# Optimization experiments

Hardware: AMD Instinct MI355X
Metric: run time of the kernel (lower is better)

Reference implementation:

```python
import jax, jax.numpy as jnp
import numpy as np

B, L, T = 256, 1024, 128

def setup_inputs() -> dict:
    key = jax.random.key(0)
    k1, k2, k3, k4 = jax.random.split(key, 4)
    inputs = jax.random.normal(k1, (B, L, T), dtype=jnp.float32)
    tag_indices = jax.random.randint(k2, (B, L), 0, T, dtype=jnp.int64)
    sequence_lengths = jax.random.randint(k3, (B,), 1, L + 1, dtype=jnp.int64)
    # xavier-ish scale for transitions
    transition_params = jax.random.normal(k4, (T, T), dtype=jnp.float32) * (2.0 / (T + T)) ** 0.5
    return {"inputs": inputs, "tag_indices": tag_indices,
            "sequence_lengths": sequence_lengths, "transition_params": transition_params}

def _crf_log_likelihood(inputs, tag_indices, sequence_lengths, transition_params):
    b, l, t = inputs.shape
    mask = (jnp.arange(l)[None, :] < sequence_lengths[:, None]).astype(inputs.dtype)  # [B,L]

    # --- unary score: sum_t inputs[b, t, tag[b,t]] over valid t ---
    unary = jnp.take_along_axis(inputs, tag_indices[:, :, None], axis=2)[:, :, 0]  # [B,L]
    unary_score = jnp.sum(unary * mask, axis=1)

    # --- binary score: sum_t trans[tag[t], tag[t+1]] masked by mask[:,1:] ---
    trans_sc = transition_params[tag_indices[:, :-1], tag_indices[:, 1:]]  # [B,L-1]
    binary_score = jnp.sum(trans_sc * mask[:, 1:], axis=1)
    sequence_scores = unary_score + binary_score

    # --- log normalizer via forward algorithm (log-space scan) ---
    first = inputs[:, 0]                               # [B,T]
    rest = jnp.transpose(inputs[:, 1:], (1, 0, 2))     # [L-1,B,T]

    def step(state, inp_t):
        # state: [B,T] previous alphas; transition broadcast: [B,T_prev,T_next]
        new = inp_t + jax.nn.logsumexp(state[:, :, None] + transition_params[None], axis=1)
        return new, new

    _, alphas = jax.lax.scan(step, first, rest)        # [L-1,B,T]
    # original indexes all_alphas at max(0, seq_len - 2)
    idx = jnp.clip(sequence_lengths - 2, 0, l - 2)
    final_alphas = alphas[idx, jnp.arange(b)]          # [B,T]
    log_norm = jax.nn.logsumexp(final_alphas, axis=1)
    log_norm = jnp.where(sequence_lengths <= 0, jnp.zeros_like(log_norm), log_norm)

    return sequence_scores - log_norm

def reference(inputs, tag_indices, sequence_lengths, transition_params):
    return _crf_log_likelihood(inputs, tag_indices, sequence_lengths, transition_params)
```

## Files before the change

### kernel.cpp

```cpp
#include <hip/hip_runtime.h>


#define B_   256
#define LL   1024
#define TT   128
#define NBLK 16
#define L2E  1.4426950408889634f
#define LN2f 0.6931471805599453f

typedef __attribute__((ext_vector_type(8))) short bf16x8;
typedef __attribute__((ext_vector_type(4))) float f32x4;
union bfrw { unsigned w[4]; bf16x8 v; };

__device__ __forceinline__ unsigned bfround(float x) {
    unsigned u = __float_as_uint(x);
    return u + 0x7fffu + ((u >> 16) & 1u);
}
__device__ __forceinline__ unsigned pack2(float lo, float hi) {
#if __has_builtin(__builtin_amdgcn_cvt_pk_bf16_f32)
    auto p = __builtin_amdgcn_cvt_pk_bf16_f32(lo, hi);
    unsigned w; __builtin_memcpy(&w, &p, 4); return w;
#else
    return __builtin_amdgcn_perm(bfround(hi), bfround(lo), 0x07060302);
#endif
}
__device__ __forceinline__ void lds_barrier() {
    asm volatile("s_waitcnt lgkmcnt(0)\n\ts_barrier" ::: "memory");
}

template<bool FWD, int PH>
__device__ __forceinline__ void phase(int t, float& Dacc, float4 (&up)[4][2],
                                      const bf16x8 (&af)[2][4],
                                      short* qls, float* sb, const float* pu,
                                      float* __restrict__ qcap, float* __restrict__ rcap,
                                      float* __restrict__ dqv, float* __restrict__ drv,
                                      int cb, int tfin, int rank,
                                      int wid, int quad, int bl)
{
    constexpr int CUR  = PH & 1;
    constexpr int NXT  = CUR ^ 1;
    constexpr int SLOT = FWD ? ((1 + PH) & 3) : ((3 - PH) & 3);

    bfrw bfr[4];
    #pragma unroll
    for (int c = 0; c < 4; ++c)
        bfr[c].v = *(const bf16x8*)(qls + CUR * (16 * 136) + bl * 136 + (4 * c + quad) * 8);
    float sprev = sb[CUR * 16 + bl];
    float ci = __builtin_amdgcn_rcpf(sprev);

    f32x4 ae0 = {0.f,0.f,0.f,0.f}, ao0 = {0.f,0.f,0.f,0.f};
    f32x4 ae1 = {0.f,0.f,0.f,0.f}, ao1 = {0.f,0.f,0.f,0.f};
    ae0 = __builtin_amdgcn_mfma_f32_16x16x32_bf16(af[0][0], bfr[0].v, ae0, 0, 0, 0);
    ae1 = __builtin_amdgcn_mfma_f32_16x16x32_bf16(af[1][0], bfr[0].v, ae1, 0, 0, 0);
    ao0 = __builtin_amdgcn_mfma_f32_16x16x32_bf16(af[0][1], bfr[1].v, ao0, 0, 0, 0);
    ao1 = __builtin_amdgcn_mfma_f32_16x16x32_bf16(af[1][1], bfr[1].v, ao1, 0, 0, 0);
    ae0 = __builtin_amdgcn_mfma_f32_16x16x32_bf16(af[0][2], bfr[2].v, ae0, 0, 0, 0);
    ae1 = __builtin_amdgcn_mfma_f32_16x16x32_bf16(af[1][2], bfr[2].v, ae1, 0, 0, 0);
    ao0 = __builtin_amdgcn_mfma_f32_16x16x32_bf16(af[0][3], bfr[3].v, ao0, 0, 0, 0);
    ao1 = __builtin_amdgcn_mfma_f32_16x16x32_bf16(af[1][3], bfr[3].v, ao1, 0, 0, 0);

    float ex[8];
    #pragma unroll
    for (int mt = 0; mt < 2; ++mt) {
        float4 v = up[SLOT][mt];
        ex[4*mt+0] = __builtin_amdgcn_exp2f(v.x * L2E);
        ex[4*mt+1] = __builtin_amdgcn_exp2f(v.y * L2E);
        ex[4*mt+2] = __builtin_amdgcn_exp2f(v.z * L2E);
        ex[4*mt+3] = __builtin_amdgcn_exp2f(v.w * L2E);
    }
    {
        int tp = FWD ? (t + 4) : (t - 5);
        tp = tp < 0 ? 0 : (tp > LL - 1 ? LL - 1 : tp);
        #pragma unroll
        for (int mt = 0; mt < 2; ++mt)
            up[SLOT][mt] = *(const float4*)(pu + (size_t)tp * TT + mt * 16);
    }
    Dacc += __builtin_amdgcn_logf(sprev);

    f32x4 s0v = ae0 + ao0;
    f32x4 s1v = ae1 + ao1;

    float rv[8];
    #pragma unroll
    for (int r = 0; r < 4; ++r) { rv[r] = ci * s0v[r]; rv[4 + r] = ci * s1v[r]; }

    if (!FWD) {
        bool cap = (cb == t - 1) && (cb != tfin);
        if (__any(cap)) {
            if (cap) {
                float4 c0 = {rv[0], rv[1], rv[2], rv[3]};
                float4 c1 = {rv[4], rv[5], rv[6], rv[7]};
                *(float4*)(rcap + rank * TT + wid * 32 + quad * 4) = c0;
                *(float4*)(rcap + rank * TT + wid * 32 + 16 + quad * 4) = c1;
                if (wid == 0 && quad == 0) drv[rank] = Dacc;
            }
        }
        bool inj = (tfin == t - 1);
        #pragma unroll
        for (int k = 0; k < 8; ++k) rv[k] = inj ? 1.0f : rv[k];
        Dacc = inj ? 0.0f : Dacc;
    }

    float ov[8];
    #pragma unroll
    for (int k = 0; k < 8; ++k) ov[k] = ex[k] * rv[k];

    if (FWD) {
        bool cap = (cb == t);
        if (__any(cap)) {
            if (cap) {
                float4 c0 = {ov[0], ov[1], ov[2], ov[3]};
                float4 c1 = {ov[4], ov[5], ov[6], ov[7]};
                *(float4*)(qcap + rank * TT + wid * 32 + quad * 4) = c0;
                *(float4*)(qcap + rank * TT + wid * 32 + 16 + quad * 4) = c1;
                if (wid == 0 && quad == 0) dqv[rank] = Dacc;
            }
        }
    }

    if (wid == 0 && quad == 0) sb[NXT * 16 + bl] = s0v[0];

    bfrw pk;
    pk.w[0] = pack2(ov[0], ov[1]);
    pk.w[1] = pack2(ov[2], ov[3]);
    pk.w[2] = pack2(ov[4], ov[5]);
    pk.w[3] = pack2(ov[6], ov[7]);
    *(bf16x8*)(qls + NXT * (16 * 136) + bl * 136 + (4 * wid + quad) * 8) = pk.v;

    lds_barrier();
}

__launch_bounds__(256, 1)
__global__ void crf_scan(const float* __restrict__ inputs,
                         const int*   __restrict__ tags,
                         const int*   __restrict__ slens,
                         const float* __restrict__ trans,
                         float* __restrict__ qcap, float* __restrict__ rcap,
                         float* __restrict__ dqv,  float* __restrict__ drv,
                         int* __restrict__ perm, float* __restrict__ scorebuf)
{
    __shared__ __align__(16) short qls[2 * 16 * 136];
    __shared__ float sb[2 * 16];
    __shared__ int keys[B_];

    const int tid  = threadIdx.x;

    if (blockIdx.x >= 2 * NBLK) {
        const int sbid = blockIdx.x - 2 * NBLK;
        const int lane = tid & 63, wid = tid >> 6;
        #pragma unroll 1
        for (int bi = 0; bi < 4; ++bi) {
            const int b = sbid * 4 + bi;
            const int slen = slens[b];
            const float* inb  = inputs + (size_t)b * LL * TT;
            const int*   tagb = tags + b * LL;
            float sc = 0.f;
            for (int t = tid; t < slen; t += 256) {
                int tg = tagb[t];
                float v = inb[(size_t)t * TT + tg];
                if (t >= 1) v += trans[tagb[t - 1] * TT + tg];
                sc += v;
            }
            #pragma unroll
            for (int off = 32; off > 0; off >>= 1) sc += __shfl_xor(sc, off, 64);
            if (lane == 0) sb[wid] = sc;
            __syncthreads();
            if (tid == 0) scorebuf[b] = sb[0] + sb[1] + sb[2] + sb[3];
            __syncthreads();
        }
        return;
    }

    const int lane = tid & 63;
    const int wid  = __builtin_amdgcn_readfirstlane(tid >> 6);
    const int quad = lane >> 4;
    const int bl   = lane & 15;
    const bool isf = (blockIdx.x < NBLK);
    const int g    = isf ? blockIdx.x : blockIdx.x - NBLK;

    keys[tid] = slens[tid] * 256 + tid;
    __syncthreads();
    for (int k = 2; k <= B_; k <<= 1) {
        for (int s = k >> 1; s > 0; s >>= 1) {
            int ixj = tid ^ s;
            if (ixj > tid) {
                int a = keys[tid], b2 = keys[ixj];
                bool asc = ((tid & k) == 0);
                if ((a > b2) == asc) { keys[tid] = b2; keys[ixj] = a; }
            }
            __syncthreads();
        }
    }
    if (isf && tid < 16) perm[g * 16 + tid] = keys[g * 16 + tid] & 255;

    const int key = keys[g * 16 + bl];
    const int ob  = key & 255;
    const int sl  = key >> 8;
    int tfin = sl - 1; if (tfin < 1) tfin = 1;

    int tmax = tfin;
    #pragma unroll
    for (int o = 1; o < 16; o <<= 1) {
        int c2 = __shfl_xor(tmax, o, 16); tmax = c2 > tmax ? c2 : tmax;
    }
    tmax = __builtin_amdgcn_readfirstlane(tmax);

    const int C  = (tmax + 4) >> 1;
    const int cb = tfin < C ? tfin : C;

    int cmax = cb, cmin = cb;
    #pragma unroll
    for (int o = 1; o < 16; o <<= 1) {
        int a = __shfl_xor(cmax, o, 16); cmax = a > cmax ? a : cmax;
        int b2 = __shfl_xor(cmin, o, 16); cmin = b2 < cmin ? b2 : cmin;
    }
    cmax = __builtin_amdgcn_readfirstlane(cmax);
    cmin = __builtin_amdgcn_readfirstlane(cmin);

    bf16x8 af[2][4];
    #pragma unroll
    for (int mt = 0; mt < 2; ++mt) {
        const int j = wid * 32 + mt * 16 + bl;
        #pragma unroll
        for (int c = 0; c < 4; ++c) {
            #pragma unroll
            for (int jj = 0; jj < 8; ++jj) {
                int k = 32 * c + 16 * (jj >> 2) + 4 * quad + (jj & 3);
                int idx = isf ? (k * TT + j) : (j * TT + k);
                float ev = __builtin_amdgcn_exp2f(trans[idx] * L2E);
                af[mt][c][jj] = (short)(bfround(ev) >> 16);
            }
        }
    }

    const float* pu = inputs + (size_t)ob * LL * TT + wid * 32 + quad * 4;
    const int rank = g * 16 + bl;
    float Dacc = 0.f;
    float4 up[4][2];

    if (tid < 16) sb[tid] = 1.0f;

    if (isf) {
        float q0[8];
        #pragma unroll
        for (int mt = 0; mt < 2; ++mt) {
            float4 v = *(const float4*)(pu + mt * 16);
            q0[4*mt+0] = __builtin_amdgcn_exp2f(v.x * L2E);
            q0[4*mt+1] = __builtin_amdgcn_exp2f(v.y * L2E);
            q0[4*mt+2] = __builtin_amdgcn_exp2f(v.z * L2E);
            q0[4*mt+3] = __builtin_amdgcn_exp2f(v.w * L2E);
        }
        bfrw pk;
        pk.w[0] = pack2(q0[0], q0[1]);
        pk.w[1] = pack2(q0[2], q0[3]);
        pk.w[2] = pack2(q0[4], q0[5]);
        pk.w[3] = pack2(q0[6], q0[7]);
        *(bf16x8*)(qls + bl * 136 + (4 * wid + quad) * 8) = pk.v;

        #pragma unroll
        for (int s = 1; s <= 4; ++s) {
            #pragma unroll
            for (int mt = 0; mt < 2; ++mt)
                up[s & 3][mt] = *(const float4*)(pu + (size_t)s * TT + mt * 16);
        }
        __syncthreads();

        for (int tb = 1; tb <= cmax; tb += 4) {
            phase<true,0>(tb+0, Dacc, up, af, qls, sb, pu, qcap, rcap, dqv, drv, cb, tfin, rank, wid, quad, bl);
            phase<true,1>(tb+1, Dacc, up, af, qls, sb, pu, qcap, rcap, dqv, drv, cb, tfin, rank, wid, quad, bl);
            phase<true,2>(tb+2, Dacc, up, af, qls, sb, pu, qcap, rcap, dqv, drv, cb, tfin, rank, wid, quad, bl);
            phase<true,3>(tb+3, Dacc, up, af, qls, sb, pu, qcap, rcap, dqv, drv, cb, tfin, rank, wid, quad, bl);
        }
    } else {
        bfrw pk;
        pk.w[0] = pk.w[1] = pk.w[2] = pk.w[3] = 0x3F803F80u;
        *(bf16x8*)(qls + bl * 136 + (4 * wid + quad) * 8) = pk.v;
        if (cb == tfin) {
            float4 one4 = {1.f, 1.f, 1.f, 1.f};
            *(float4*)(rcap + rank * TT + wid * 32 + quad * 4) = one4;
            *(float4*)(rcap + rank * TT + wid * 32 + 16 + quad * 4) = one4;
            if (wid == 0 && quad == 0) drv[rank] = 0.f;
        }

        const int tb0 = (tmax + 4) & ~3;
        #pragma unroll
        for (int ph = 0; ph < 4; ++ph) {
            int ui = tb0 - 1 - ph;
            ui = ui > LL - 1 ? LL - 1 : (ui < 0 ? 0 : ui);
            #pragma unroll
            for (int mt = 0; mt < 2; ++mt)
                up[(3 - ph) & 3][mt] = *(const float4*)(pu + (size_t)ui * TT + mt * 16);
        }
        __syncthreads();

        for (int tb = tb0; tb > cmin; tb -= 4) {
            phase<false,0>(tb-0, Dacc, up, af, qls, sb, pu, qcap, rcap, dqv, drv, cb, tfin, rank, wid, quad, bl);
            phase<false,1>(tb-1, Dacc, up, af, qls, sb, pu, qcap, rcap, dqv, drv, cb, tfin, rank, wid, quad, bl);
            phase<false,2>(tb-2, Dacc, up, af, qls, sb, pu, qcap, rcap, dqv, drv, cb, tfin, rank, wid, quad, bl);
            phase<false,3>(tb-3, Dacc, up, af, qls, sb, pu, qcap, rcap, dqv, drv, cb, tfin, rank, wid, quad, bl);
        }
    }
}

__global__ void crf_comb(const float* __restrict__ qcap, const float* __restrict__ rcap,
                         const float* __restrict__ dqv, const float* __restrict__ drv,
                         const int* __restrict__ perm, const float* __restrict__ scorebuf,
                         float* __restrict__ out) {
    const int tid = threadIdx.x;
    const int r16 = tid >> 4, part = tid & 15;
    const int rank = blockIdx.x * 16 + r16;
    const float* qc = qcap + rank * TT + part * 8;
    const float* rc = rcap + rank * TT + part * 8;
    float4 a0 = *(const float4*)(qc);
    float4 a1 = *(const float4*)(qc + 4);
    float4 b0 = *(const float4*)(rc);
    float4 b1 = *(const float4*)(rc + 4);
    float s = a0.x*b0.x + a0.y*b0.y + a0.z*b0.z + a0.w*b0.w
            + a1.x*b1.x + a1.y*b1.y + a1.z*b1.z + a1.w*b1.w;
    #pragma unroll
    for (int o = 1; o < 16; o <<= 1) s += __shfl_xor(s, o, 16);
    if (part == 0) {
        int ob = perm[rank];
        float logZ = LN2f * (__builtin_amdgcn_logf(s) + dqv[rank] + drv[rank]);
        out[ob] = scorebuf[ob] - logZ;
    }
}

extern "C" void kernel_launch(void* const* d_in, const int* in_sizes, int n_in,
                              void* d_out, int out_size, void* d_ws, size_t ws_size,
                              hipStream_t stream) {
    const float* inputs = (const float*)d_in[0];
    const int*   tags   = (const int*)d_in[1];
    const int*   slens  = (const int*)d_in[2];
    const float* trans  = (const float*)d_in[3];
    float* out = (float*)d_out;

    float* qcap = (float*)d_ws;
    float* rcap = qcap + 32768;
    float* dqv  = rcap + 32768;
    float* drv  = dqv + 256;
    int*   perm = (int*)(drv + 256);
    float* scorebuf = (float*)(perm + 256);

    crf_scan<<<2 * NBLK + 64, 256, 0, stream>>>(inputs, tags, slens, trans,
                                                qcap, rcap, dqv, drv, perm, scorebuf);
    crf_comb<<<NBLK, 256, 0, stream>>>(qcap, rcap, dqv, drv, perm, scorebuf, out);
}
```

Baseline: 410.3 us.

## Run one single-wave block per sequence with fp16 register matvec instead of MFMA

Replaces the 16-sequence-per-block MFMA scan, which needed a sort by length and a 4-wave LDS barrier every step, with 512 single-wavefront blocks, one per sequence and direction. Each lane keeps two columns of exp(transitions) as packed fp16 in registers and computes the matvec with scalar fp16-to-fp32 FMAs, so steps need only an LDS waitcnt and no s_barrier. Each block also stops at its own sequence's meet point rather than the group maximum. The score work is spread over 256 one-wave blocks. The cost is about 128 FMAs per lane per step on the vector ALUs instead of matrix cores, heavy register pressure from the 128-entry E array, and fp16 range and precision risk in the scaled alphas.

Result: slower. 743.9 us (+81.3%).

```diff
diff --git a/kernel.cpp b/kernel.cpp
--- a/kernel.cpp
+++ b/kernel.cpp
@@ -1,316 +1,232 @@
 #include <hip/hip_runtime.h>
 
 
-#define B_   256
 #define LL   1024
 #define TT   128
-#define NBLK 16
 #define L2E  1.4426950408889634f
 #define LN2f 0.6931471805599453f
 
-typedef __attribute__((ext_vector_type(8))) short bf16x8;
-typedef __attribute__((ext_vector_type(4))) float f32x4;
-union bfrw { unsigned w[4]; bf16x8 v; };
-
-__device__ __forceinline__ unsigned bfround(float x) {
-    unsigned u = __float_as_uint(x);
-    return u + 0x7fffu + ((u >> 16) & 1u);
-}
-__device__ __forceinline__ unsigned pack2(float lo, float hi) {
-#if __has_builtin(__builtin_amdgcn_cvt_pk_bf16_f32)
-    auto p = __builtin_amdgcn_cvt_pk_bf16_f32(lo, hi);
-    unsigned w; __builtin_memcpy(&w, &p, 4); return w;
+typedef __attribute__((ext_vector_type(2))) __fp16 h2;
+typedef __attribute__((ext_vector_type(2))) float f2;
+union h2u { h2 h; unsigned u; };
+
+__device__ __forceinline__ h2 pkh(float lo, float hi) {
+#if __has_builtin(__builtin_amdgcn_cvt_pkrtz)
+    return __builtin_amdgcn_cvt_pkrtz(lo, hi);
 #else
-    return __builtin_amdgcn_perm(bfround(hi), bfround(lo), 0x07060302);
+    h2 r; r.x = (__fp16)lo; r.y = (__fp16)hi; return r;
 #endif
 }
-__device__ __forceinline__ void lds_barrier() {
-    asm volatile("s_waitcnt lgkmcnt(0)\n\ts_barrier" ::: "memory");
+__device__ __forceinline__ float dmix(h2 a, h2 b, float c) {
+    c += (float)a.x * (float)b.x;
+    c += (float)a.y * (float)b.y;
+    return c;
 }
 
 template<bool FWD, int PH>
-__device__ __forceinline__ void phase(int t, float& Dacc, float4 (&up)[4][2],
-                                      const bf16x8 (&af)[2][4],
-                                      short* qls, float* sb, const float* pu,
-                                      float* __restrict__ qcap, float* __restrict__ rcap,
-                                      float* __restrict__ dqv, float* __restrict__ drv,
-                                      int cb, int tfin, int rank,
-                                      int wid, int quad, int bl)
+__device__ __forceinline__ void step1(int t, float& Dacc, f2 (&up)[4],
+                                      const h2 (&E)[64][2],
+                                      unsigned (&lds)[2][128],
+                                      const float* pu,
+                                      float* capg, float* dcapg,
+                                      int cb, int tfin, int lane)
 {
     constexpr int CUR  = PH & 1;
     constexpr int NXT  = CUR ^ 1;
     constexpr int SLOT = FWD ? ((1 + PH) & 3) : ((3 - PH) & 3);
 
-    bfrw bfr[4];
-    #pragma unroll
-    for (int c = 0; c < 4; ++c)
-        bfr[c].v = *(const bf16x8*)(qls + CUR * (16 * 136) + bl * 136 + (4 * c + quad) * 8);
-    float sprev = sb[CUR * 16 + bl];
-    float ci = __builtin_amdgcn_rcpf(sprev);
-
-    f32x4 ae0 = {0.f,0.f,0.f,0.f}, ao0 = {0.f,0.f,0.f,0.f};
-    f32x4 ae1 = {0.f,0.f,0.f,0.f}, ao1 = {0.f,0.f,0.f,0.f};
-    ae0 = __builtin_amdgcn_mfma_f32_16x16x32_bf16(af[0][0], bfr[0].v, ae0, 0, 0, 0);
-    ae1 = __builtin_amdgcn_mfma_f32_16x16x32_bf16(af[1][0], bfr[0].v, ae1, 0, 0, 0);
-    ao0 = __builtin_amdgcn_mfma_f32_16x16x32_bf16(af[0][1], bfr[1].v, ao0, 0, 0, 0);
-    ao1 = __builtin_amdgcn_mfma_f32_16x16x32_bf16(af[1][1], bfr[1].v, ao1, 0, 0, 0);
-    ae0 = __builtin_amdgcn_mfma_f32_16x16x32_bf16(af[0][2], bfr[2].v, ae0, 0, 0, 0);
-    ae1 = __builtin_amdgcn_mfma_f32_16x16x32_bf16(af[1][2], bfr[2].v, ae1, 0, 0, 0);
-    ao0 = __builtin_amdgcn_mfma_f32_16x16x32_bf16(af[0][3], bfr[3].v, ao0, 0, 0, 0);
-    ao1 = __builtin_amdgcn_mfma_f32_16x16x32_bf16(af[1][3], bfr[3].v, ao1, 0, 0, 0);
-
-    float ex[8];
-    #pragma unroll
-    for (int mt = 0; mt < 2; ++mt) {
-        float4 v = up[SLOT][mt];
-        ex[4*mt+0] = __builtin_amdgcn_exp2f(v.x * L2E);
-        ex[4*mt+1] = __builtin_amdgcn_exp2f(v.y * L2E);
-        ex[4*mt+2] = __builtin_amdgcn_exp2f(v.z * L2E);
-        ex[4*mt+3] = __builtin_amdgcn_exp2f(v.w * L2E);
-    }
+    float sprev = __uint_as_float(lds[CUR][64]);
+    const uint4* sp = (const uint4*)&lds[CUR][0];
+
+    float ex0 = __builtin_amdgcn_exp2f(up[SLOT].x * L2E);
+    float ex1 = __builtin_amdgcn_exp2f(up[SLOT].y * L2E);
     {
         int tp = FWD ? (t + 4) : (t - 5);
         tp = tp < 0 ? 0 : (tp > LL - 1 ? LL - 1 : tp);
-        #pragma unroll
-        for (int mt = 0; mt < 2; ++mt)
-            up[SLOT][mt] = *(const float4*)(pu + (size_t)tp * TT + mt * 16);
-    }
-    Dacc += __builtin_amdgcn_logf(sprev);
-
-    f32x4 s0v = ae0 + ao0;
-    f32x4 s1v = ae1 + ao1;
-
-    float rv[8];
+        up[SLOT] = *(const f2*)(pu + (size_t)tp * TT);
+    }
+
+    float a[4] = {0.f, 0.f, 0.f, 0.f};
+    float c[4] = {0.f, 0.f, 0.f, 0.f};
     #pragma unroll
-    for (int r = 0; r < 4; ++r) { rv[r] = ci * s0v[r]; rv[4 + r] = ci * s1v[r]; }
+    for (int g = 0; g < 4; ++g) {
+        #pragma unroll
+        for (int r = 0; r < 4; ++r) {
+            uint4 wv = sp[4 * g + r];
+            const int k0 = g * 16 + r * 4;
+            h2u u0, u1, u2, u3;
+            u0.u = wv.x; u1.u = wv.y; u2.u = wv.z; u3.u = wv.w;
+            a[g] = dmix(E[k0+0][0], u0.h, a[g]);
+            c[g] = dmix(E[k0+0][1], u0.h, c[g]);
+            a[g] = dmix(E[k0+1][0], u1.h, a[g]);
+            c[g] = dmix(E[k0+1][1], u1.h, c[g]);
+            a[g] = dmix(E[k0+2][0], u2.h, a[g]);
+            c[g] = dmix(E[k0+2][1], u2.h, c[g]);
+            a[g] = dmix(E[k0+3][0], u3.h, a[g]);
+            c[g] = dmix(E[k0+3][1], u3.h, c[g]);
+        }
+    }
+    float s0 = (a[0] + a[1]) + (a[2] + a[3]);
+    float s1 = (c[0] + c[1]) + (c[2] + c[3]);
+
+    float ci = __builtin_amdgcn_rcpf(sprev);
+    float lg = __builtin_amdgcn_logf(sprev);
+    bool inj = (!FWD) && (tfin == t - 1);
+    float cis  = inj ? 0.f : ci;
+    float injf = inj ? 1.f : 0.f;
+    Dacc = inj ? 0.f : (Dacc + lg);
+
+    float rv0 = cis * s0 + injf;
+    float rv1 = cis * s1 + injf;
 
     if (!FWD) {
-        bool cap = (cb == t - 1) && (cb != tfin);
-        if (__any(cap)) {
-            if (cap) {
-                float4 c0 = {rv[0], rv[1], rv[2], rv[3]};
-                float4 c1 = {rv[4], rv[5], rv[6], rv[7]};
-                *(float4*)(rcap + rank * TT + wid * 32 + quad * 4) = c0;
-                *(float4*)(rcap + rank * TT + wid * 32 + 16 + quad * 4) = c1;
-                if (wid == 0 && quad == 0) drv[rank] = Dacc;
-            }
-        }
-        bool inj = (tfin == t - 1);
-        #pragma unroll
-        for (int k = 0; k < 8; ++k) rv[k] = inj ? 1.0f : rv[k];
-        Dacc = inj ? 0.0f : Dacc;
-    }
-
-    float ov[8];
-    #pragma unroll
-    for (int k = 0; k < 8; ++k) ov[k] = ex[k] * rv[k];
+        if (cb == t - 1 && cb != tfin) {
+            f2 cp; cp.x = rv0; cp.y = rv1;
+            *(f2*)(capg + 2 * lane) = cp;
+            if (lane == 0) *dcapg = Dacc;
+        }
+    }
+
+    float ov0 = ex0 * rv0;
+    float ov1 = ex1 * rv1;
 
     if (FWD) {
-        bool cap = (cb == t);
-        if (__any(cap)) {
-            if (cap) {
-                float4 c0 = {ov[0], ov[1], ov[2], ov[3]};
-                float4 c1 = {ov[4], ov[5], ov[6], ov[7]};
-                *(float4*)(qcap + rank * TT + wid * 32 + quad * 4) = c0;
-                *(float4*)(qcap + rank * TT + wid * 32 + 16 + quad * 4) = c1;
-                if (wid == 0 && quad == 0) dqv[rank] = Dacc;
-            }
-        }
-    }
-
-    if (wid == 0 && quad == 0) sb[NXT * 16 + bl] = s0v[0];
-
-    bfrw pk;
-    pk.w[0] = pack2(ov[0], ov[1]);
-    pk.w[1] = pack2(ov[2], ov[3]);
-    pk.w[2] = pack2(ov[4], ov[5]);
-    pk.w[3] = pack2(ov[6], ov[7]);
-    *(bf16x8*)(qls + NXT * (16 * 136) + bl * 136 + (4 * wid + quad) * 8) = pk.v;
-
-    lds_barrier();
-}
-
-__launch_bounds__(256, 1)
+        if (cb == t) {
+            f2 cp; cp.x = ov0; cp.y = ov1;
+            *(f2*)(capg + 2 * lane) = cp;
+            if (lane == 0) *dcapg = Dacc;
+        }
+    }
+
+    h2u pk; pk.h = pkh(ov0, ov1);
+    lds[NXT][lane] = pk.u;
+    if (lane == 0) lds[NXT][64] = __float_as_uint(s0);
+    asm volatile("s_waitcnt lgkmcnt(0)" ::: "memory");
+}
+
+__launch_bounds__(64, 1)
 __global__ void crf_scan(const float* __restrict__ inputs,
                          const int*   __restrict__ tags,
                          const int*   __restrict__ slens,
                          const float* __restrict__ trans,
                          float* __restrict__ qcap, float* __restrict__ rcap,
                          float* __restrict__ dqv,  float* __restrict__ drv,
-                         int* __restrict__ perm, float* __restrict__ scorebuf)
+                         float* __restrict__ scorebuf)
 {
-    __shared__ __align__(16) short qls[2 * 16 * 136];
-    __shared__ float sb[2 * 16];
-    __shared__ int keys[B_];
-
-    const int tid  = threadIdx.x;
-
-    if (blockIdx.x >= 2 * NBLK) {
-        const int sbid = blockIdx.x - 2 * NBLK;
-        const int lane = tid & 63, wid = tid >> 6;
+    const int bid  = blockIdx.x;
+    const int lane = threadIdx.x;
+
+    if (bid >= 512) {
+        const int b = bid - 512;
+        const int slen = slens[b];
+        const float* inb  = inputs + (size_t)b * LL * TT;
+        const int*   tagb = tags + b * LL;
+        float sc = 0.f;
+        for (int t = lane; t < slen; t += 64) {
+            int tg = tagb[t];
+            float v = inb[(size_t)t * TT + tg];
+            if (t >= 1) v += trans[tagb[t - 1] * TT + tg];
+            sc += v;
+        }
+        #pragma unroll
+        for (int off = 32; off > 0; off >>= 1) sc += __shfl_xor(sc, off, 64);
+        if (lane == 0) scorebuf[b] = sc;
+        return;
+    }
+
+    __shared__ __align__(16) unsigned lds[2][128];
+
+    const bool isf = bid < 256;
+    const int  b   = isf ? bid : bid - 256;
+
+    int sl = slens[b];
+    int tfin = sl - 1; if (tfin < 1) tfin = 1;
+    const int cb = (tfin + 1) >> 1;
+
+    h2 E[64][2];
+    if (isf) {
+        #pragma unroll
+        for (int kk = 0; kk < 64; ++kk) {
+            f2 r0 = *(const f2*)(trans + (size_t)(2 * kk)     * TT + 2 * lane);
+            f2 r1 = *(const f2*)(trans + (size_t)(2 * kk + 1) * TT + 2 * lane);
+            E[kk][0] = pkh(__builtin_amdgcn_exp2f(r0.x * L2E),
+                           __builtin_amdgcn_exp2f(r1.x * L2E));
+            E[kk][1] = pkh(__builtin_amdgcn_exp2f(r0.y * L2E),
+                           __builtin_amdgcn_exp2f(r1.y * L2E));
+        }
+    } else {
+        #pragma unroll
+        for (int jj = 0; jj < 64; ++jj) {
+            f2 r0 = *(const f2*)(trans + (size_t)(2 * lane)     * TT + 2 * jj);
+            f2 r1 = *(const f2*)(trans + (size_t)(2 * lane + 1) * TT + 2 * jj);
+            E[jj][0] = pkh(__builtin_amdgcn_exp2f(r0.x * L2E),
+                           __builtin_amdgcn_exp2f(r0.y * L2E));
+            E[jj][1] = pkh(__builtin_amdgcn_exp2f(r1.x * L2E),
+                           __builtin_amdgcn_exp2f(r1.y * L2E));
+        }
+    }
+
+    const float* pu = inputs + (size_t)b * LL * TT + 2 * lane;
+    float Dacc = 0.f;
+    f2 up[4];
+
+    if (isf) {
+        f2 v0 = *(const f2*)(pu);
+        h2u pk0;
+        pk0.h = pkh(__builtin_amdgcn_exp2f(v0.x * L2E),
+                    __builtin_amdgcn_exp2f(v0.y * L2E));
+        lds[0][lane] = pk0.u;
+        if (lane == 0) lds[0][64] = __float_as_uint(1.0f);
+        #pragma unroll
+        for (int s = 1; s <= 4; ++s)
+            up[s & 3] = *(const f2*)(pu + (size_t)s * TT);
+        asm volatile("s_waitcnt lgkmcnt(0)" ::: "memory");
+
+        float* capg = qcap + (size_t)b * TT;
         #pragma unroll 1
-        for (int bi = 0; bi < 4; ++bi) {
-            const int b = sbid * 4 + bi;
-            const int slen = slens[b];
-            const float* inb  = inputs + (size_t)b * LL * TT;
-            const int*   tagb = tags + b * LL;
-            float sc = 0.f;
-            for (int t = tid; t < slen; t += 256) {
-                int tg = tagb[t];
-                float v = inb[(size_t)t * TT + tg];
-                if (t >= 1) v += trans[tagb[t - 1] * TT + tg];
-                sc += v;
-            }
-            #pragma unroll
-            for (int off = 32; off > 0; off >>= 1) sc += __shfl_xor(sc, off, 64);
-            if (lane == 0) sb[wid] = sc;
-            __syncthreads();
-            if (tid == 0) scorebuf[b] = sb[0] + sb[1] + sb[2] + sb[3];
-            __syncthreads();
-        }
-        return;
-    }
-
-    const int lane = tid & 63;
-    const int wid  = __builtin_amdgcn_readfirstlane(tid >> 6);
-    const int quad = lane >> 4;
-    const int bl   = lane & 15;
-    const bool isf = (blockIdx.x < NBLK);
-    const int g    = isf ? blockIdx.x : blockIdx.x - NBLK;
-
-    keys[tid] = slens[tid] * 256 + tid;
-    __syncthreads();
-    for (int k = 2; k <= B_; k <<= 1) {
-        for (int s = k >> 1; s > 0; s >>= 1) {
-            int ixj = tid ^ s;
-            if (ixj > tid) {
-                int a = keys[tid], b2 = keys[ixj];
-                bool asc = ((tid & k) == 0);
-                if ((a > b2) == asc) { keys[tid] = b2; keys[ixj] = a; }
-            }
-            __syncthreads();
-        }
-    }
-    if (isf && tid < 16) perm[g * 16 + tid] = keys[g * 16 + tid] & 255;
-
-    const int key = keys[g * 16 + bl];
-    const int ob  = key & 255;
-    const int sl  = key >> 8;
-    int tfin = sl - 1; if (tfin < 1) tfin = 1;
-
-    int tmax = tfin;
-    #pragma unroll
-    for (int o = 1; o < 16; o <<= 1) {
-        int c2 = __shfl_xor(tmax, o, 16); tmax = c2 > tmax ? c2 : tmax;
-    }
-    tmax = __builtin_amdgcn_readfirstlane(tmax);
-
-    const int C  = (tmax + 4) >> 1;
-    const int cb = tfin < C ? tfin : C;
-
-    int cmax = cb, cmin = cb;
-    #pragma unroll
-    for (int o = 1; o < 16; o <<= 1) {
-        int a = __shfl_xor(cmax, o, 16); cmax = a > cmax ? a : cmax;
-        int b2 = __shfl_xor(cmin, o, 16); cmin = b2 < cmin ? b2 : cmin;
-    }
-    cmax = __builtin_amdgcn_readfirstlane(cmax);
-    cmin = __builtin_amdgcn_readfirstlane(cmin);
-
-    bf16x8 af[2][4];
-    #pragma unroll
-    for (int mt = 0; mt < 2; ++mt) {
-        const int j = wid * 32 + mt * 16 + bl;
-        #pragma unroll
-        for (int c = 0; c < 4; ++c) {
-            #pragma unroll
-            for (int jj = 0; jj < 8; ++jj) {
-                int k = 32 * c + 16 * (jj >> 2) + 4 * quad + (jj & 3);
-                int idx = isf ? (k * TT + j) : (j * TT + k);
-                float ev = __builtin_amdgcn_exp2f(trans[idx] * L2E);
-                af[mt][c][jj] = (short)(bfround(ev) >> 16);
-            }
-        }
-    }
-
-    const float* pu = inputs + (size_t)ob * LL * TT + wid * 32 + quad * 4;
-    const int rank = g * 16 + bl;
-    float Dacc = 0.f;
-    float4 up[4][2];
-
-    if (tid < 16) sb[tid] = 1.0f;
-
-    if (isf) {
-        float q0[8];
-        #pragma unroll
-        for (int mt = 0; mt < 2; ++mt) {
-            float4 v = *(const float4*)(pu + mt * 16);
-            q0[4*mt+0] = __builtin_amdgcn_exp2f(v.x * L2E);
-            q0[4*mt+1] = __builtin_amdgcn_exp2f(v.y * L2E);
-            q0[4*mt+2] = __builtin_amdgcn_exp2f(v.z * L2E);
-            q0[4*mt+3] = __builtin_amdgcn_exp2f(v.w * L2E);
-        }
-        bfrw pk;
-        pk.w[0] = pack2(q0[0], q0[1]);
-        pk.w[1] = pack2(q0[2], q0[3]);
-        pk.w[2] = pack2(q0[4], q0[5]);
-        pk.w[3] = pack2(q0[6], q0[7]);
-        *(bf16x8*)(qls + bl * 136 + (4 * wid + quad) * 8) = pk.v;
-
-        #pragma unroll
-        for (int s = 1; s <= 4; ++s) {
-            #pragma unroll
-            for (int mt = 0; mt < 2; ++mt)
-                up[s & 3][mt] = *(const float4*)(pu + (size_t)s * TT + mt * 16);
-        }
-        __syncthreads();
-
-        for (int tb = 1; tb <= cmax; tb += 4) {
-            phase<true,0>(tb+0, Dacc, up, af, qls, sb, pu, qcap, rcap, dqv, drv, cb, tfin, rank, wid, quad, bl);
-            phase<true,1>(tb+1, Dacc, up, af, qls, sb, pu, qcap, rcap, dqv, drv, cb, tfin, rank, wid, quad, bl);
-            phase<true,2>(tb+2, Dacc, up, af, qls, sb, pu, qcap, rcap, dqv, drv, cb, tfin, rank, wid, quad, bl);
-            phase<true,3>(tb+3, Dacc, up, af, qls, sb, pu, qcap, rcap, dqv, drv, cb, tfin, rank, wid, quad, bl);
+        for (int tb = 1; tb <= cb; tb += 4) {
+            step1<true,0>(tb+0, Dacc, up, E, lds, pu, capg, dqv + b, cb, tfin, lane);
+            step1<true,1>(tb+1, Dacc, up, E, lds, pu, capg, dqv + b, cb, tfin, lane);
+            step1<true,2>(tb+2, Dacc, up, E, lds, pu, capg, dqv + b, cb, tfin, lane);
+            step1<true,3>(tb+3, Dacc, up, E, lds, pu, capg, dqv + b, cb, tfin, lane);
         }
     } else {
-        bfrw pk;
-        pk.w[0] = pk.w[1] = pk.w[2] = pk.w[3] = 0x3F803F80u;
-        *(bf16x8*)(qls + bl * 136 + (4 * wid + quad) * 8) = pk.v;
+        lds[0][lane] = 0x3C003C00u;
+        if (lane == 0) lds[0][64] = __float_as_uint(1.0f);
         if (cb == tfin) {
-            float4 one4 = {1.f, 1.f, 1.f, 1.f};
-            *(float4*)(rcap + rank * TT + wid * 32 + quad * 4) = one4;
-            *(float4*)(rcap + rank * TT + wid * 32 + 16 + quad * 4) = one4;
-            if (wid == 0 && quad == 0) drv[rank] = 0.f;
-        }
-
-        const int tb0 = (tmax + 4) & ~3;
+            f2 one2; one2.x = 1.f; one2.y = 1.f;
+            *(f2*)(rcap + (size_t)b * TT + 2 * lane) = one2;
+            if (lane == 0) drv[b] = 0.f;
+        }
+        const int tb0 = (tfin + 4) & ~3;
         #pragma unroll
         for (int ph = 0; ph < 4; ++ph) {
             int ui = tb0 - 1 - ph;
             ui = ui > LL - 1 ? LL - 1 : (ui < 0 ? 0 : ui);
-            #pragma unroll
-            for (int mt = 0; mt < 2; ++mt)
-                up[(3 - ph) & 3][mt] = *(const float4*)(pu + (size_t)ui * TT + mt * 16);
-        }
-        __syncthreads();
-
-        for (int tb = tb0; tb > cmin; tb -= 4) {
-            phase<false,0>(tb-0, Dacc, up, af, qls, sb, pu, qcap, rcap, dqv, drv, cb, tfin, rank, wid, quad, bl);
-            phase<false,1>(tb-1, Dacc, up, af, qls, sb, pu, qcap, rcap, dqv, drv, cb, tfin, rank, wid, quad, bl);
-            phase<false,2>(tb-2, Dacc, up, af, qls, sb, pu, qcap, rcap, dqv, drv, cb, tfin, rank, wid, quad, bl);
-            phase<false,3>(tb-3, Dacc, up, af, qls, sb, pu, qcap, rcap, dqv, drv, cb, tfin, rank, wid, quad, bl);
+            up[(3 - ph) & 3] = *(const f2*)(pu + (size_t)ui * TT);
+        }
+        asm volatile("s_waitcnt lgkmcnt(0)" ::: "memory");
+
+        float* capg = rcap + (size_t)b * TT;
+        #pragma unroll 1
+        for (int tb = tb0; tb > cb; tb -= 4) {
+            step1<false,0>(tb-0, Dacc, up, E, lds, pu, capg, drv + b, cb, tfin, lane);
+            step1<false,1>(tb-1, Dacc, up, E, lds, pu, capg, drv + b, cb, tfin, lane);
+            step1<false,2>(tb-2, Dacc, up, E, lds, pu, capg, drv + b, cb, tfin, lane);
+            step1<false,3>(tb-3, Dacc, up, E, lds, pu, capg, drv + b, cb, tfin, lane);
         }
     }
 }
 
 __global__ void crf_comb(const float* __restrict__ qcap, const float* __restrict__ rcap,
                          const float* __restrict__ dqv, const float* __restrict__ drv,
-                         const int* __restrict__ perm, const float* __restrict__ scorebuf,
+                         const float* __restrict__ scorebuf,
                          float* __restrict__ out) {
     const int tid = threadIdx.x;
     const int r16 = tid >> 4, part = tid & 15;
-    const int rank = blockIdx.x * 16 + r16;
-    const float* qc = qcap + rank * TT + part * 8;
-    const float* rc = rcap + rank * TT + part * 8;
+    const int b = blockIdx.x * 16 + r16;
+    const float* qc = qcap + (size_t)b * TT + part * 8;
+    const float* rc = rcap + (size_t)b * TT + part * 8;
     float4 a0 = *(const float4*)(qc);
     float4 a1 = *(const float4*)(qc + 4);
     float4 b0 = *(const float4*)(rc);
@@ -320,9 +236,8 @@
     #pragma unroll
     for (int o = 1; o < 16; o <<= 1) s += __shfl_xor(s, o, 16);
     if (part == 0) {
-        int ob = perm[rank];
-        float logZ = LN2f * (__builtin_amdgcn_logf(s) + dqv[rank] + drv[rank]);
-        out[ob] = scorebuf[ob] - logZ;
+        float logZ = LN2f * (__builtin_amdgcn_logf(s) + dqv[b] + drv[b]);
+        out[b] = scorebuf[b] - logZ;
     }
 }
 
@@ -339,10 +254,9 @@
     float* rcap = qcap + 32768;
     float* dqv  = rcap + 32768;
     float* drv  = dqv + 256;
-    int*   perm = (int*)(drv + 256);
-    float* scorebuf = (float*)(perm + 256);
-
-    crf_scan<<<2 * NBLK + 64, 256, 0, stream>>>(inputs, tags, slens, trans,
-                                                qcap, rcap, dqv, drv, perm, scorebuf);
-    crf_comb<<<NBLK, 256, 0, stream>>>(qcap, rcap, dqv, drv, perm, scorebuf, out);
-}
+    float* scorebuf = drv + 256;
+
+    crf_scan<<<768, 64, 0, stream>>>(inputs, tags, slens, trans,
+                                     qcap, rcap, dqv, drv, scorebuf);
+    crf_comb<<<16, 256, 0, stream>>>(qcap, rcap, dqv, drv, scorebuf, out);
+}
```
